# Performance work log

Hardware: AMD Instinct MI355X
Metric: run time of the kernel (lower is better)

Reference implementation:

```python
import jax, jax.numpy as jnp
import numpy as np

B, M, D, H = 8, 1024, 512, 8


def setup_inputs() -> dict:
    key = jax.random.key(0)
    ks = jax.random.split(key, 8)
    s = 0.02
    return {
        'x': jax.random.normal(ks[0], (B, M, D), jnp.float32),
        'scale': jnp.ones((M, D), jnp.float32),
        'Wq': jax.random.normal(ks[1], (H, D, D), jnp.float32) * s,
        'Wk': jax.random.normal(ks[2], (H, D, D), jnp.float32) * s,
        'Wv': jax.random.normal(ks[3], (H, D, D), jnp.float32) * s,
        'Wo': jax.random.normal(ks[4], (D, H * D), jnp.float32) * s,
        'bo': jnp.zeros((D,), jnp.float32),
        'Wff': jax.random.normal(ks[5], (D, D), jnp.float32) * s,
        'bff': jnp.zeros((D,), jnp.float32),
        'Wg': jax.random.normal(ks[6], (D, D), jnp.float32) * s,
        'bg': jnp.zeros((D,), jnp.float32),
        'Wl': jax.random.normal(ks[7], (D, D), jnp.float32) * s,
        'bl': jnp.zeros((D,), jnp.float32),
        'beta': jnp.ones((1,), jnp.float32),
    }


def _rope_cos_sin(m, d):
    # theta = 10000 ** (-2*(i-1)/d), faithful to the original (note the i-1 quirk)
    i = jnp.arange(d // 2, dtype=jnp.float32)
    theta = jnp.power(10000.0, -2.0 * (i - 1.0) / d)
    ang = jnp.arange(m, dtype=jnp.float32)[:, None] * theta[None, :]  # [m, d/2]
    return jnp.cos(ang), jnp.sin(ang)


def _apply_rope(t, cos, sin):
    # t: [..., m, d]; equivalent to bmm with the block-diagonal rotation matrix R[p]
    te, to = t[..., 0::2], t[..., 1::2]
    re = te * cos + to * sin
    ro = -te * sin + to * cos
    return jnp.stack([re, ro], axis=-1).reshape(t.shape)


def _rmsnorm(x, scale):
    b, m, d = x.shape
    ff_rms = jnp.sqrt(jnp.sum(x * x, axis=(1, 2))) * (m * d) ** (-0.5)  # [b]
    return scale[None, :m, :] * (x / ff_rms[:, None, None])


def reference(x, scale, Wq, Wk, Wv, Wo, bo, Wff, bff, Wg, bg, Wl, bl, beta):
    b, m, d = x.shape
    xn = _rmsnorm(x, scale)

    # per-head full-width projections (nn.Linear: y = x @ W.T)
    q = jnp.einsum('bmd,hod->hbmo', xn, Wq)  # [H,B,M,D]
    k = jnp.einsum('bmd,hod->hbmo', xn, Wk)
    v = jnp.einsum('bmd,hod->hbmo', xn, Wv)

    cos, sin = _rope_cos_sin(m, d)
    qr = _apply_rope(q, cos, sin)
    kr = _apply_rope(k, cos, sin)

    # SDPA with is_causal=False (no mask); dropout disabled (eval)
    scores = jnp.einsum('hbqd,hbkd->hbqk', qr, kr) / jnp.sqrt(jnp.float32(d))
    attn = jax.nn.softmax(scores, axis=-1)
    ctx = jnp.einsum('hbqk,hbkd->hbqd', attn, v)  # [H,B,M,D]

    cat = jnp.transpose(ctx, (1, 2, 0, 3)).reshape(b, m, -1)  # [B,M,H*D]
    attn_out = cat @ Wo.T + bo

    x2 = xn + attn_out
    x3 = _rmsnorm(x2, scale)

    h1 = x3 @ Wff.T + bff
    g = h1 @ Wg.T + bg
    sw = g * jax.nn.sigmoid(beta * g)
    ff = sw * (h1 @ Wl.T + bl)
    return x3 + ff
```

## Files before the change

kernel.cpp:

```cpp
#include <hip/hip_runtime.h>
#include <math.h>

typedef unsigned short u16;
typedef float f32x4 __attribute__((ext_vector_type(4)));
typedef __bf16 bf16x8 __attribute__((ext_vector_type(8)));
typedef unsigned short u16x8 __attribute__((ext_vector_type(8)));

__device__ __forceinline__ float bf2f(u16 u) {
    union { float f; unsigned int i; } v; v.i = ((unsigned int)u) << 16; return v.f;
}
__device__ __forceinline__ u16 f2bf(float f) {
    union { float f; unsigned int i; } v; v.f = f;
    unsigned int r = v.i + 0x7fffu + ((v.i >> 16) & 1u);
    return (u16)(r >> 16);
}
__device__ __forceinline__ float dpp_swap1(float v) {
    union { float f; int i; } a, b; a.f = v;
    b.i = __builtin_amdgcn_update_dpp(0, a.i, 0xB1, 0xF, 0xF, true);
    return b.f;
}

__device__ __forceinline__ void gll(const u16* g, u16* l) {
    __builtin_amdgcn_global_load_lds((const __attribute__((address_space(1))) void*)g,
                                     (__attribute__((address_space(3))) void*)l, 16, 0, 0);
}

struct EpiBF16 {
    u16* C; long zs; int ldc;
    __device__ void operator()(int z, int m, int n, float v) const {
        C[(long)z * zs + (long)m * ldc + n] = f2bf(v);
    }
};
struct EpiScale {
    u16* C; long zs; int ldc; float s;
    __device__ void operator()(int z, int m, int n, float v) const {
        C[(long)z * zs + (long)m * ldc + n] = f2bf(v * s);
    }
};
struct EpiAcc {
    float* x2;
    __device__ void operator()(int z, int m, int n, float v) const {
        x2[(long)m * 512 + n] += v;
    }
};
struct EpiBias16 {
    u16* C; const float* bias;
    __device__ void operator()(int z, int m, int n, float v) const {
        C[(long)m * 512 + n] = f2bf(v + bias[n]);
    }
};
struct EpiGL {
    u16* g; u16* l; const float* bg; const float* bl;
    __device__ void operator()(int z, int m, int n, float v) const {
        if (n < 512) g[(long)m * 512 + n] = f2bf(v + bg[n]);
        else         l[(long)m * 512 + n - 512] = f2bf(v + bl[n - 512]);
    }
};
struct EpiCtxMul {
    u16* C; const float* rs;
    __device__ void operator()(int z, int m, int n, float v) const {
        float r = __builtin_amdgcn_rcpf(rs[(long)z * 1024 + m]);
        C[(long)z * 524288 + (long)m * 512 + n] = f2bf(v * r);
    }
};

struct EpiScores {
    u16* C; float* rs; float sscale;
    __device__ float elem(int z, int m, int n, float v) const {
        float e = __expf(v * sscale);
        C[(long)z * 1048576 + (long)m * 1024 + n] = f2bf(e);
        return e;
    }
    __device__ void row(int z, int m, float p, int l15) const {
        p += __shfl_xor(p, 1, 64); p += __shfl_xor(p, 2, 64);
        p += __shfl_xor(p, 4, 64); p += __shfl_xor(p, 8, 64);
        if (l15 == 0) atomicAdd(rs + (long)z * 1024 + m, p);
    }
};
struct EpiAccA {
    float* x2;
    __device__ float elem(int z, int m, int n, float v) const {
        atomicAdd(x2 + (long)m * 512 + n, v);
        return 0.f;
    }
    __device__ void row(int, int, float, int) const {}
};

#define RDA(S, I) (*(const bf16x8*)(lds + (S) * 8192 + (I) * 512 + aro))
#define RDB(S, J) (*(const bf16x8*)(lds + (S) * 8192 + (J) * 512 + bro))
#define MFMA_PH(JP) do { \
    __builtin_amdgcn_s_barrier(); \
    asm volatile("s_waitcnt lgkmcnt(0)" ::: "memory"); \
    __builtin_amdgcn_sched_barrier(0); \
    __builtin_amdgcn_s_setprio(1); \
    _Pragma("unroll") \
    for (int i_ = 0; i_ < 8; i_++) { \
        acc[i_][2*(JP)]   = __builtin_amdgcn_mfma_f32_16x16x32_bf16(aF[i_], bF[0], acc[i_][2*(JP)], 0, 0, 0); \
        acc[i_][2*(JP)+1] = __builtin_amdgcn_mfma_f32_16x16x32_bf16(aF[i_], bF[1], acc[i_][2*(JP)+1], 0, 0, 0); \
    } \
    __builtin_amdgcn_s_setprio(0); \
} while (0)

__launch_bounds__(512, 2)
__global__ void gemm256_qkv(const u16* __restrict__ xnb, const u16* __restrict__ Wqkv,
                            u16* __restrict__ q, u16* __restrict__ k, u16* __restrict__ vT,
                            const float* __restrict__ csT) {
    __shared__ __align__(16) u16 lds[65536];
    const int t = threadIdx.x;
    const int lane = t & 63, wave = t >> 6;
    const int wr = wave >> 2, wc = wave & 3;
    const int l15 = lane & 15, quad = lane >> 4;
    const int sr = t >> 2;
    const int scw = ((t & 3) ^ ((t >> 3) & 3)) * 8;
    u16* lA0 = lds + wave * 512 + lane * 8;
    u16* lB0 = lds + 32768 + wave * 512 + lane * 8;
    const int ap = (quad ^ ((l15 >> 1) & 3)) * 8;
    const int aro = (wr * 128 + l15) * 32 + ap;
    const int bro = 32768 + (wc * 64 + l15) * 32 + ap;
    const int bid = blockIdx.x;

    const u16 *curA, *curB, *nxtA, *nxtB;
    int cm0, cn0, cz, cmode, nm0, nn0, nz, nmode;
    auto decode = [&](int tid, const u16*& A_, const u16*& B_,
                      int& m0_, int& n0_, int& z_, int& md_) {
        if (tid > 1535) tid = 1535;
        if (tid < 1024) {
            md_ = 0; z_ = tid & 15; int rem = tid >> 4;
            m0_ = (rem >> 1) << 8; n0_ = (rem & 1) << 8;
            A_ = xnb + (long)(m0_ + sr) * 512 + scw;
            B_ = Wqkv + z_ * 262144 + (long)(n0_ + sr) * 512 + scw;
        } else {
            int v = tid - 1024; md_ = 1; z_ = v & 7; int rem = v >> 3;
            m0_ = (rem & 1) << 8; n0_ = (rem >> 1) << 8;
            A_ = Wqkv + 4194304 + z_ * 262144 + (long)(m0_ + sr) * 512 + scw;
            B_ = xnb + (long)(n0_ + sr) * 512 + scw;
        }
    };
    decode(bid, curA, curB, cm0, cn0, cz, cmode);
    decode(bid + 256, nxtA, nxtB, nm0, nn0, nz, nmode);

    auto STGA = [&](int s) {
        const u16* base = (s < 16) ? curA : nxtA;
        int c = (s < 16) ? s : s - 16;
        u16* d = lA0 + (s & 3) * 8192;
        const u16* src = base + c * 32;
        gll(src, d); gll(src + 65536, d + 4096);
    };
    auto STGB = [&](int s) {
        const u16* base = (s < 16) ? curB : nxtB;
        int c = (s < 16) ? s : s - 16;
        u16* d = lB0 + (s & 3) * 8192;
        const u16* src = base + c * 32;
        gll(src, d); gll(src + 65536, d + 4096);
    };

    STGA(0); STGB(0); STGA(1); STGB(1); STGA(2); STGB(2);
    asm volatile("s_waitcnt vmcnt(4)" ::: "memory");
    __builtin_amdgcn_s_barrier();

    for (int j = 0; j < 6; ++j) {
        f32x4 acc[8][4] = {};
        #pragma unroll
        for (int it = 0; it < 4; ++it) {
            const int sh = 3 + it * 4;
            bf16x8 aF[8], bF[2];
            #pragma unroll
            for (int i = 0; i < 8; i++) aF[i] = RDA(0, i);
            bF[0] = RDB(0, 0); bF[1] = RDB(0, 1);
            STGA(sh);
            MFMA_PH(0);
            __builtin_amdgcn_s_barrier();
            bF[0] = RDB(0, 2); bF[1] = RDB(0, 3);
            STGB(sh);
            MFMA_PH(1);
            __builtin_amdgcn_s_barrier();
            #pragma unroll
            for (int i = 0; i < 8; i++) aF[i] = RDA(1, i);
            bF[0] = RDB(1, 0); bF[1] = RDB(1, 1);
            STGA(sh + 1);
            MFMA_PH(0);
            __builtin_amdgcn_s_barrier();
            bF[0] = RDB(1, 2); bF[1] = RDB(1, 3);
            STGB(sh + 1);
            MFMA_PH(1);
            asm volatile("s_waitcnt vmcnt(4)" ::: "memory");
            __builtin_amdgcn_s_barrier();
            #pragma unroll
            for (int i = 0; i < 8; i++) aF[i] = RDA(2, i);
            bF[0] = RDB(2, 0); bF[1] = RDB(2, 1);
            STGA(sh + 2);
            MFMA_PH(0);
            __builtin_amdgcn_s_barrier();
            bF[0] = RDB(2, 2); bF[1] = RDB(2, 3);
            STGB(sh + 2);
            MFMA_PH(1);
            __builtin_amdgcn_s_barrier();
            #pragma unroll
            for (int i = 0; i < 8; i++) aF[i] = RDA(3, i);
            bF[0] = RDB(3, 0); bF[1] = RDB(3, 1);
            STGA(sh + 3);
            MFMA_PH(0);
            __builtin_amdgcn_s_barrier();
            bF[0] = RDB(3, 2); bF[1] = RDB(3, 3);
            STGB(sh + 3);
            MFMA_PH(1);
            asm volatile("s_waitcnt vmcnt(4)" ::: "memory");
            __builtin_amdgcn_s_barrier();
        }
        if (cmode == 0) {
            u16* dst = ((cz >= 8) ? k : q) + ((long)(cz & 7) << 22);
            const int odd = l15 & 1;
            #pragma unroll
            for (int i = 0; i < 8; i++)
                #pragma unroll
                for (int r = 0; r < 4; r++) {
                    int m = cm0 + wr * 128 + i * 16 + quad * 4 + r;
                    const float* cs = csT + (long)(m & 1023) * 512;
                    #pragma unroll
                    for (int jj = 0; jj < 4; jj++) {
                        int n = cn0 + wc * 64 + jj * 16 + l15;
                        float val = acc[i][jj][r];
                        float pv = dpp_swap1(val);
                        float c = cs[(n >> 1) * 2], s = cs[(n >> 1) * 2 + 1];
                        float o = odd ? (val * c - pv * s) : (val * c + pv * s);
                        dst[(long)m * 512 + n] = f2bf(o);
                    }
                }
        } else {
            #pragma unroll
            for (int i = 0; i < 8; i++)
                #pragma unroll
                for (int r = 0; r < 4; r++) {
                    int m = cm0 + wr * 128 + i * 16 + quad * 4 + r;
                    #pragma unroll
                    for (int jj = 0; jj < 4; jj++) {
                        int n = cn0 + wc * 64 + jj * 16 + l15;
                        vT[((long)cz << 22) + ((long)(n >> 10) << 19) + ((long)m << 10) + (n & 1023)]
                            = f2bf(acc[i][jj][r]);
                    }
                }
        }
        curA = nxtA; curB = nxtB; cm0 = nm0; cn0 = nn0; cz = nz; cmode = nmode;
        decode(bid + (j + 2) * 256, nxtA, nxtB, nm0, nn0, nz, nmode);
    }
    asm volatile("s_waitcnt vmcnt(0)" ::: "memory");
}

template <class Epi>
__launch_bounds__(512, 2)
__global__ void gemm256(const u16* __restrict__ A, const u16* __restrict__ B,
                        int nkh, int kssh, int lda, int ldb,
                        long aBatch, long bBatch, long aSeg, long bSeg, Epi epi) {
    __shared__ __align__(16) u16 lds[65536];
    const int t = threadIdx.x;
    const int lane = t & 63, wave = t >> 6;
    const int wr = wave >> 2, wc = wave & 3;
    const int l15 = lane & 15, quad = lane >> 4;
    const int m0 = blockIdx.x * 256, n0 = blockIdx.y * 256;
    const int z = blockIdx.z;
    const int sr = t >> 2;
    const int scw = ((t & 3) ^ ((t >> 3) & 3)) * 8;
    const u16* gA = A + (long)z * aBatch + (long)(m0 + sr) * lda + scw;
    const u16* gB = B + (long)z * bBatch + (long)(n0 + sr) * ldb + scw;
    const long a128 = 128L * lda, b128 = 128L * ldb;
    u16* lA0 = lds + wave * 512 + lane * 8;
    u16* lB0 = lds + 32768 + wave * 512 + lane * 8;
    const int kmask = (1 << kssh) - 1;

    auto STA = [&](int shp) {
        int c = shp < nkh ? shp : nkh - 1;
        const u16* s = gA + (long)(c >> kssh) * aSeg + (c & kmask) * 32;
        u16* d = lA0 + (shp & 3) * 8192;
        gll(s, d); gll(s + a128, d + 4096);
    };
    auto STB = [&](int shp) {
        int c = shp < nkh ? shp : nkh - 1;
        const u16* s = gB + (long)(c >> kssh) * bSeg + (c & kmask) * 32;
        u16* d = lB0 + (shp & 3) * 8192;
        gll(s, d); gll(s + b128, d + 4096);
    };

    const int ap = (quad ^ ((l15 >> 1) & 3)) * 8;
    const int aro = (wr * 128 + l15) * 32 + ap;
    const int bro = 32768 + (wc * 64 + l15) * 32 + ap;
    f32x4 acc[8][4] = {};

    STA(0); STB(0); STA(1); STB(1); STA(2); STB(2);
    asm volatile("s_waitcnt vmcnt(4)" ::: "memory");
    __builtin_amdgcn_s_barrier();

    const int niter = nkh >> 2;
    int sh = 3;
    for (int it = 0; it < niter; it++) {
        bf16x8 aF[8], bF[2];
        #pragma unroll
        for (int i = 0; i < 8; i++) aF[i] = RDA(0, i);
        bF[0] = RDB(0, 0); bF[1] = RDB(0, 1);
        STA(sh);
        MFMA_PH(0);
        __builtin_amdgcn_s_barrier();
        bF[0] = RDB(0, 2); bF[1] = RDB(0, 3);
        STB(sh);
        MFMA_PH(1);
        __builtin_amdgcn_s_barrier();
        #pragma unroll
        for (int i = 0; i < 8; i++) aF[i] = RDA(1, i);
        bF[0] = RDB(1, 0); bF[1] = RDB(1, 1);
        STA(sh + 1);
        MFMA_PH(0);
        __builtin_amdgcn_s_barrier();
        bF[0] = RDB(1, 2); bF[1] = RDB(1, 3);
        STB(sh + 1);
        MFMA_PH(1);
        asm volatile("s_waitcnt vmcnt(4)" ::: "memory");
        __builtin_amdgcn_s_barrier();
        #pragma unroll
        for (int i = 0; i < 8; i++) aF[i] = RDA(2, i);
        bF[0] = RDB(2, 0); bF[1] = RDB(2, 1);
        STA(sh + 2);
        MFMA_PH(0);
        __builtin_amdgcn_s_barrier();
        bF[0] = RDB(2, 2); bF[1] = RDB(2, 3);
        STB(sh + 2);
        MFMA_PH(1);
        __builtin_amdgcn_s_barrier();
        #pragma unroll
        for (int i = 0; i < 8; i++) aF[i] = RDA(3, i);
        bF[0] = RDB(3, 0); bF[1] = RDB(3, 1);
        STA(sh + 3);
        MFMA_PH(0);
        __builtin_amdgcn_s_barrier();
        bF[0] = RDB(3, 2); bF[1] = RDB(3, 3);
        STB(sh + 3);
        MFMA_PH(1);
        asm volatile("s_waitcnt vmcnt(4)" ::: "memory");
        __builtin_amdgcn_s_barrier();
        sh += 4;
    }
    asm volatile("s_waitcnt vmcnt(0)" ::: "memory");

    #pragma unroll
    for (int i = 0; i < 8; i++)
        #pragma unroll
        for (int r = 0; r < 4; r++) {
            int m = m0 + wr * 128 + i * 16 + quad * 4 + r;
            float p = 0.f;
            #pragma unroll
            for (int j = 0; j < 4; j++)
                p += epi.elem(z, m, n0 + wc * 64 + j * 16 + l15, acc[i][j][r]);
            epi.row(z, m, p, l15);
        }
}
#undef RDA
#undef RDB
#undef MFMA_PH

template <class Epi>
__launch_bounds__(256, 4)
__global__ void gemm128(const u16* __restrict__ A, const u16* __restrict__ B,
                        int Kseg, int nSeg, int lda, int ldb,
                        long aBatch, long bBatch, long aSeg, Epi epi) {
    __shared__ __align__(16) u16 sA[8192];
    __shared__ __align__(16) u16 sB[8192];
    const int t = threadIdx.x;
    const int lane = t & 63, wave = t >> 6;
    const int wr = wave >> 1, wc = wave & 1;
    const int l15 = lane & 15, quad = lane >> 4;
    const int m0 = blockIdx.x * 128, n0 = blockIdx.y * 128;
    const int sr = t >> 2;
    const int scw = ((t & 3) ^ ((t >> 3) & 3)) * 8;
    const u16* gA = A + (long)blockIdx.z * aBatch + (long)(m0 + sr) * lda + scw;
    const u16* gB = B + (long)blockIdx.z * bBatch + (long)(n0 + sr) * ldb + scw;
    const long a2 = 64L * lda, b2 = 64L * ldb;
    u16* lA = sA + wave * 512 + lane * 8;
    u16* lB = sB + wave * 512 + lane * 8;
    const int ap = (quad ^ ((l15 >> 1) & 3)) * 8;
    const int ab = (wr * 64 + l15) * 32 + ap;
    const int bb = (wc * 64 + l15) * 32 + ap;
    f32x4 acc[4][4] = {};
    for (int s = 0; s < nSeg; s++) {
        const u16* gAs = gA + (long)s * aSeg;
        const u16* gBs = gB + s * Kseg;
        for (int k0 = 0; k0 < Kseg; k0 += 64) {
            gll(gAs + k0, lA);             gll(gAs + k0 + a2, lA + 2048);
            gll(gBs + k0, lB);             gll(gBs + k0 + b2, lB + 2048);
            gll(gAs + k0 + 32, lA + 4096); gll(gAs + k0 + 32 + a2, lA + 6144);
            gll(gBs + k0 + 32, lB + 4096); gll(gBs + k0 + 32 + b2, lB + 6144);
            __syncthreads();
            #pragma unroll
            for (int half = 0; half < 2; half++) {
                bf16x8 aF[4], bF[4];
                #pragma unroll
                for (int i = 0; i < 4; i++) aF[i] = *(const bf16x8*)(sA + half * 4096 + ab + i * 512);
                #pragma unroll
                for (int j = 0; j < 4; j++) bF[j] = *(const bf16x8*)(sB + half * 4096 + bb + j * 512);
                #pragma unroll
                for (int i = 0; i < 4; i++)
                    #pragma unroll
                    for (int j = 0; j < 4; j++)
                        acc[i][j] = __builtin_amdgcn_mfma_f32_16x16x32_bf16(aF[i], bF[j], acc[i][j], 0, 0, 0);
            }
            __syncthreads();
        }
    }
    #pragma unroll
    for (int i = 0; i < 4; i++)
        #pragma unroll
        for (int j = 0; j < 4; j++)
            #pragma unroll
            for (int r = 0; r < 4; r++)
                epi(blockIdx.z, m0 + wr * 64 + i * 16 + quad * 4 + r,
                    n0 + wc * 64 + j * 16 + l15, acc[i][j][r]);
}

__device__ __forceinline__ float waveSum(float v) {
    #pragma unroll
    for (int o = 32; o > 0; o >>= 1) v += __shfl_down(v, o, 64);
    return v;
}
__device__ __forceinline__ float invFromPart(const float* part, int b) {
    float s = part[b * 64 + (threadIdx.x & 63)];
    s = waveSum(s);
    s = __shfl(s, 0, 64);
    return sqrtf(524288.0f / s);
}

__global__ void sumsq_f32(const float* __restrict__ x, float* __restrict__ part) {
    __shared__ float tmp[4];
    long base = (long)blockIdx.x * 524288 + (long)blockIdx.y * 8192;
    float s = 0.f;
    for (int i = threadIdx.x; i < 8192; i += 256) { float v = x[base + i]; s += v * v; }
    s = waveSum(s);
    if ((threadIdx.x & 63) == 0) tmp[threadIdx.x >> 6] = s;
    __syncthreads();
    if (threadIdx.x == 0) part[blockIdx.x * 64 + blockIdx.y] = tmp[0] + tmp[1] + tmp[2] + tmp[3];
}
__global__ void finalize_inv(const float* __restrict__ part, float* __restrict__ inv) {
    float s = part[blockIdx.x * 64 + threadIdx.x];
    s = waveSum(s);
    if (threadIdx.x == 0) inv[blockIdx.x] = sqrtf(524288.0f / s);
}
__global__ void rmsnorm1f_a(const float* __restrict__ x, const float* __restrict__ scale,
                            const float* __restrict__ part, const float* __restrict__ bo,
                            u16* __restrict__ xnb, float* __restrict__ x2) {
    long i = (long)blockIdx.x * 256 + threadIdx.x;
    int b = (int)(i >> 19), md = (int)(i & 524287);
    float inv = invFromPart(part, b);
    float v = x[i] * inv * scale[md];
    xnb[i] = f2bf(v);
    x2[i] = v + bo[i & 511];
}
__global__ void rmsnorm2_a(const float* __restrict__ x2, const float* __restrict__ scale,
                           const float* __restrict__ part, u16* __restrict__ x3b) {
    long i = (long)blockIdx.x * 256 + threadIdx.x;
    int b = (int)(i >> 19), md = (int)(i & 524287);
    float inv = invFromPart(part, b);
    x3b[i] = f2bf(x2[i] * inv * scale[md]);
}
__global__ void final_out_a(const float* __restrict__ x2, const float* __restrict__ scale,
                            const float* __restrict__ part, const u16* __restrict__ g,
                            const u16* __restrict__ l, const float* __restrict__ beta,
                            float* __restrict__ out) {
    long i = (long)blockIdx.x * 256 + threadIdx.x;
    int b = (int)(i >> 19), md = (int)(i & 524287);
    float inv2 = invFromPart(part, b);
    float x3 = x2[i] * inv2 * scale[md];
    float gv = bf2f(g[i]), lv = bf2f(l[i]);
    float bta = beta[0];
    float sw = gv / (1.0f + expf(-bta * gv));
    out[i] = x3 + sw * lv;
}
__global__ void rmsnorm1f(const float* __restrict__ x, const float* __restrict__ scale,
                          const float* __restrict__ inv, const float* __restrict__ bo,
                          u16* __restrict__ xnb, float* __restrict__ x2) {
    long i = (long)blockIdx.x * 256 + threadIdx.x;
    int b = (int)(i >> 19), md = (int)(i & 524287);
    float v = x[i] * inv[b] * scale[md];
    xnb[i] = f2bf(v);
    x2[i] = v + bo[i & 511];
}
__global__ void rmsnorm2(const float* __restrict__ x2, const float* __restrict__ scale,
                         const float* __restrict__ inv, u16* __restrict__ x3b) {
    long i = (long)blockIdx.x * 256 + threadIdx.x;
    int b = (int)(i >> 19), md = (int)(i & 524287);
    x3b[i] = f2bf(x2[i] * inv[b] * scale[md]);
}
__global__ void final_out(const float* __restrict__ x2, const float* __restrict__ scale,
                          const float* __restrict__ inv2, const u16* __restrict__ g,
                          const u16* __restrict__ l, const float* __restrict__ beta,
                          float* __restrict__ out) {
    long i = (long)blockIdx.x * 256 + threadIdx.x;
    int b = (int)(i >> 19), md = (int)(i & 524287);
    float x3 = x2[i] * inv2[b] * scale[md];
    float gv = bf2f(g[i]), lv = bf2f(l[i]);
    float bta = beta[0];
    float sw = gv / (1.0f + expf(-bta * gv));
    out[i] = x3 + sw * lv;
}
__global__ void rope_tables_a(float* __restrict__ csT, float* __restrict__ rowsum) {
    int i = blockIdx.x * 256 + threadIdx.x;
    int m = i >> 8, j = i & 255;
    float theta = powf(10000.0f, -2.0f * ((float)j - 1.0f) / 512.0f);
    float ang = (float)m * theta;
    csT[2 * i] = cosf(ang); csT[2 * i + 1] = sinf(ang);
    if (i < 65536) rowsum[i] = 0.f;
}
__global__ void rope_tables(float* __restrict__ cosT, float* __restrict__ sinT) {
    int i = blockIdx.x * 256 + threadIdx.x;
    int m = i >> 8, j = i & 255;
    float theta = powf(10000.0f, -2.0f * ((float)j - 1.0f) / 512.0f);
    float ang = (float)m * theta;
    cosT[i] = cosf(ang); sinT[i] = sinf(ang);
}
__global__ void rope_apply(u16* __restrict__ tq, const float* __restrict__ cosT,
                           const float* __restrict__ sinT) {
    long i = (long)blockIdx.x * 256 + threadIdx.x;
    int j = (int)(i & 255), m = (int)((i >> 8) & 1023);
    float c = cosT[m * 256 + j], s = sinT[m * 256 + j];
    long base = i * 2;
    float te = bf2f(tq[base]), to = bf2f(tq[base + 1]);
    tq[base]     = f2bf(te * c + to * s);
    tq[base + 1] = f2bf(-te * s + to * c);
}
__global__ void transpose_v(const u16* __restrict__ v, u16* __restrict__ vT) {
    __shared__ u16 tile[32][33];
    long zb = (long)blockIdx.z * 524288;
    int mo = blockIdx.x * 32, oo = blockIdx.y * 32;
    int tx = threadIdx.x & 31, ty = threadIdx.x >> 5;
    for (int r = ty; r < 32; r += 8) tile[r][tx] = v[zb + (long)(mo + r) * 512 + oo + tx];
    __syncthreads();
    for (int r = ty; r < 32; r += 8) vT[zb + (long)(oo + r) * 1024 + mo + tx] = tile[tx][r];
}
__launch_bounds__(256)
__global__ void softmax_rows4(u16* __restrict__ sc) {
    int row = blockIdx.x * 4 + (threadIdx.x >> 6);
    int lane = threadIdx.x & 63;
    u16* p = sc + (long)row * 1024 + lane * 16;
    float v[16]; float mx = -1e30f;
    #pragma unroll
    for (int i = 0; i < 16; i++) { v[i] = bf2f(p[i]); mx = fmaxf(mx, v[i]); }
    #pragma unroll
    for (int o = 32; o > 0; o >>= 1) mx = fmaxf(mx, __shfl_xor(mx, o, 64));
    float s = 0.f;
    #pragma unroll
    for (int i = 0; i < 16; i++) { v[i] = expf(v[i] - mx); s += v[i]; }
    #pragma unroll
    for (int o = 32; o > 0; o >>= 1) s += __shfl_xor(s, o, 64);
    float r = 1.0f / s;
    #pragma unroll
    for (int i = 0; i < 16; i++) p[i] = f2bf(v[i] * r);
}
__device__ __forceinline__ void cvt8(const float* __restrict__ s, u16* __restrict__ d) {
    f32x4 a = *(const f32x4*)s, b = *(const f32x4*)(s + 4);
    u16x8 o;
    o[0] = f2bf(a[0]); o[1] = f2bf(a[1]); o[2] = f2bf(a[2]); o[3] = f2bf(a[3]);
    o[4] = f2bf(b[0]); o[5] = f2bf(b[1]); o[6] = f2bf(b[2]); o[7] = f2bf(b[3]);
    *(u16x8*)d = o;
}
__global__ void prep_w(const float* __restrict__ Wq, const float* __restrict__ Wk,
                       const float* __restrict__ Wv, const float* __restrict__ Wo,
                       const float* __restrict__ Wff, const float* __restrict__ Wg,
                       const float* __restrict__ Wl,
                       u16* __restrict__ Wqkvb, u16* __restrict__ Wob,
                       u16* __restrict__ Wffb, u16* __restrict__ Wglb) {
    long i = ((long)blockIdx.x * 256 + threadIdx.x) * 8;
    if (i < 2097152)      cvt8(Wq + i, Wqkvb + i);
    else if (i < 4194304) cvt8(Wk + (i - 2097152), Wqkvb + i);
    else if (i < 6291456) cvt8(Wv + (i - 4194304), Wqkvb + i);
    else if (i < 8388608) cvt8(Wo + (i - 6291456), Wob + (i - 6291456));
    else if (i < 8650752) cvt8(Wff + (i - 8388608), Wffb + (i - 8388608));
    else if (i < 8912896) cvt8(Wg + (i - 8650752), Wglb + (i - 8650752));
    else                  cvt8(Wl + (i - 8912896), Wglb + 262144 + (i - 8912896));
}
__global__ void convert_f2b(const float* __restrict__ s, u16* __restrict__ d, int n) {
    int i = blockIdx.x * 256 + threadIdx.x;
    if (i < n) d[i] = f2bf(s[i]);
}
__global__ void convert3(const float* __restrict__ a, const float* __restrict__ b,
                         const float* __restrict__ c, u16* __restrict__ d) {
    int i = blockIdx.x * 256 + threadIdx.x;
    const float* s = (i < 262144) ? a : (i < 524288) ? b : c;
    d[i] = f2bf(s[i & 262143]);
}

#define MB 1048576L
extern "C" void kernel_launch(void* const* d_in, const int* in_sizes, int n_in,
                              void* d_out, int out_size, void* d_ws, size_t ws_size,
                              hipStream_t stream) {
    (void)in_sizes; (void)n_in; (void)out_size;
    const float* x    = (const float*)d_in[0];
    const float* scale= (const float*)d_in[1];
    const float* Wq   = (const float*)d_in[2];
    const float* Wk   = (const float*)d_in[3];
    const float* Wv   = (const float*)d_in[4];
    const float* Wo   = (const float*)d_in[5];
    const float* bo   = (const float*)d_in[6];
    const float* Wff  = (const float*)d_in[7];
    const float* bff  = (const float*)d_in[8];
    const float* Wg   = (const float*)d_in[9];
    const float* bg   = (const float*)d_in[10];
    const float* Wl   = (const float*)d_in[11];
    const float* bl   = (const float*)d_in[12];
    const float* beta = (const float*)d_in[13];
    float* out = (float*)d_out;
    char* ws = (char*)d_ws;
    const float sscale = 0.044194173824159216f;

    if (ws_size >= 260000000UL) {
        u16*   xnb   = (u16*)  (ws);
        u16*   q_all = (u16*)  (ws + 8*MB);
        u16*   k_all = (u16*)  (ws + 72*MB);
        u16*   vT_all= (u16*)  (ws + 136*MB);
        u16*   sc    = (u16*)  (ws + 200*MB);
        u16*   Wqkvb = (u16*)  (ws + 200*MB);
        u16*   Wob   = (u16*)  (ws + 232*MB);
        u16*   Wffb  = (u16*)  (ws + 236*MB);
        u16*   Wglb  = (u16*)  (ws + 236*MB + 524288L);
        float* csT   = (float*)(ws + 237*MB + 1572864L);
        float* rowsum= (float*)(ws + 239*MB + 1572864L);
        float* part  = (float*)(ws + 239*MB + 1835008L);
        float* x2    = out;
        u16* x3b = k_all; u16* h1 = k_all + 4194304; u16* g = k_all + 8388608; u16* l = k_all + 12582912;

        sumsq_f32<<<dim3(8, 64), 256, 0, stream>>>(x, part);
        rmsnorm1f_a<<<16384, 256, 0, stream>>>(x, scale, part, bo, xnb, x2);
        rope_tables_a<<<1024, 256, 0, stream>>>(csT, rowsum);
        prep_w<<<4480, 256, 0, stream>>>(Wq, Wk, Wv, Wo, Wff, Wg, Wl,
                                         Wqkvb, Wob, Wffb, Wglb);

        gemm256_qkv<<<256, 512, 0, stream>>>(xnb, Wqkvb, q_all, k_all, vT_all, csT);

        for (int h0 = 0; h0 < 8; h0 += 2) {
            const long off = (long)h0 * 4194304;
            float* rsc = rowsum + (long)h0 * 8192;
            gemm256<<<dim3(4, 4, 16), 512, 0, stream>>>(q_all + off, k_all + off, 16, 4, 512, 512,
                524288L, 524288L, 512L, 512L, EpiScores{sc, rsc, sscale});
            gemm128<<<dim3(8, 4, 16), 256, 0, stream>>>(sc, vT_all + off, 1024, 1, 1024, 1024,
                1048576L, 524288L, 0L, EpiCtxMul{q_all + off, rsc});
        }
        gemm256<<<dim3(32, 2, 4), 512, 0, stream>>>(q_all, Wob, 32, 4, 512, 4096,
            8388608L, 1024L, 4194304L, 512L, EpiAccA{x2});

        sumsq_f32<<<dim3(8, 64), 256, 0, stream>>>(x2, part);
        rmsnorm2_a<<<16384, 256, 0, stream>>>(x2, scale, part, x3b);

        gemm128<<<dim3(64, 4, 1), 256, 0, stream>>>(x3b, Wffb, 512, 1, 512, 512,
            0L, 0L, 0L, EpiBias16{h1, bff});
        gemm128<<<dim3(64, 8, 1), 256, 0, stream>>>(h1, Wglb, 512, 1, 512, 512,
            0L, 0L, 0L, EpiGL{g, l, bg, bl});
        final_out_a<<<16384, 256, 0, stream>>>(x2, scale, part, g, l, beta, out);
        return;
    }

    u16*   xnb  = (u16*)  (ws);
    float* x2   = (float*)(ws + 8388608L);
    u16*   qh   = (u16*)  (ws + 25165824L);
    u16*   kh   = (u16*)  (ws + 33554432L);
    u16*   vhc  = (u16*)  (ws + 41943040L);
    u16*   vT   = (u16*)  (ws + 50331648L);
    u16*   Whb  = (u16*)  (ws + 58720256L);
    u16*   Wob  = (u16*)  (ws + 60293120L);
    u16*   Wfb  = (u16*)  (ws + 64487424L);
    u16*   Wgb  = (u16*)  (ws + 65011712L);
    u16*   Wlb  = (u16*)  (ws + 65536000L);
    float* cosT = (float*)(ws + 66060288L);
    float* sinT = (float*)(ws + 67108864L);
    float* part = (float*)(ws + 68157440L);
    float* inv1 = (float*)(ws + 68159488L);
    float* inv2 = (float*)(ws + 68159552L);
    u16*   sc   = (u16*)  (ws + 68159616L);
    u16*   x3b = qh;  u16* h1 = kh;  u16* g = vhc;  u16* l = vT;
    const bool big = ws_size >= 85002240UL;

    sumsq_f32<<<dim3(8, 64), 256, 0, stream>>>(x, part);
    finalize_inv<<<8, 64, 0, stream>>>(part, inv1);
    rmsnorm1f<<<16384, 256, 0, stream>>>(x, scale, inv1, bo, xnb, x2);
    rope_tables<<<1024, 256, 0, stream>>>(cosT, sinT);
    convert_f2b<<<8192, 256, 0, stream>>>(Wo, Wob, 2097152);
    convert_f2b<<<1024, 256, 0, stream>>>(Wff, Wfb, 262144);
    convert_f2b<<<1024, 256, 0, stream>>>(Wg, Wgb, 262144);
    convert_f2b<<<1024, 256, 0, stream>>>(Wl, Wlb, 262144);

    for (int h = 0; h < 8; h++) {
        convert3<<<3072, 256, 0, stream>>>(Wq + (long)h * 262144, Wk + (long)h * 262144,
                                           Wv + (long)h * 262144, Whb);
        gemm128<<<dim3(64, 4, 3), 256, 0, stream>>>(xnb, Whb, 512, 1, 512, 512, 0L, 262144L, 0L,
                                                    EpiBF16{qh, 4194304L, 512});
        rope_apply<<<16384, 256, 0, stream>>>(qh, cosT, sinT);
        transpose_v<<<dim3(32, 16, 8), 256, 0, stream>>>(vhc, vT);
        if (big) {
            gemm128<<<dim3(8, 8, 8), 256, 0, stream>>>(qh, kh, 512, 1, 512, 512, 524288L, 524288L,
                                                       0L, EpiScale{sc, 1048576L, 1024, sscale});
            softmax_rows4<<<2048, 256, 0, stream>>>(sc);
            gemm128<<<dim3(8, 4, 8), 256, 0, stream>>>(sc, vT, 1024, 1, 1024, 1024, 1048576L,
                                                       524288L, 0L, EpiBF16{vhc, 524288L, 512});
        } else {
            for (int b = 0; b < 8; b++) {
                gemm128<<<dim3(8, 8, 1), 256, 0, stream>>>(qh + (long)b * 524288, kh + (long)b * 524288,
                                                           512, 1, 512, 512, 0L, 0L, 0L,
                                                           EpiScale{sc, 0L, 1024, sscale});
                softmax_rows4<<<256, 256, 0, stream>>>(sc);
                gemm128<<<dim3(8, 4, 1), 256, 0, stream>>>(sc, vT + (long)b * 524288, 1024, 1, 1024,
                                                           1024, 0L, 0L, 0L,
                                                           EpiBF16{vhc + (long)b * 524288, 0L, 512});
            }
        }
        gemm128<<<dim3(64, 4, 1), 256, 0, stream>>>(vhc, Wob + (long)h * 512, 512, 1, 512, 4096,
                                                    0L, 0L, 0L, EpiAcc{x2});
    }

    sumsq_f32<<<dim3(8, 64), 256, 0, stream>>>(x2, part);
    finalize_inv<<<8, 64, 0, stream>>>(part, inv2);
    rmsnorm2<<<16384, 256, 0, stream>>>(x2, scale, inv2, x3b);
    gemm128<<<dim3(64, 4, 1), 256, 0, stream>>>(x3b, Wfb, 512, 1, 512, 512, 0L, 0L, 0L,
                                                EpiBias16{h1, bff});
    gemm128<<<dim3(64, 4, 1), 256, 0, stream>>>(h1, Wgb, 512, 1, 512, 512, 0L, 0L, 0L,
                                                EpiBias16{g, bg});
    gemm128<<<dim3(64, 4, 1), 256, 0, stream>>>(h1, Wlb, 512, 1, 512, 512, 0L, 0L, 0L,
                                                EpiBias16{l, bl});
    final_out<<<16384, 256, 0, stream>>>(x2, scale, inv2, g, l, beta, out);
}
```

Measured before the change: 643.1 us.

## Pack GEMM epilogue stores, replace atomic split-K with partials, vectorize elementwise kernels

GEMM epilogues now pair adjacent columns with a DPP swap, so even lanes write two bf16 values (or two floats) as one 32/64-bit store instead of two scalar stores. The Wo split-K GEMM writes per-split partial buffers instead of doing float atomicAdds into x2. A new combine kernel sums those partials into x2 and computes the sum of squares in the same pass, which removes the separate sumsq launch. The rmsnorm and final elementwise kernels process four elements per thread with vector loads and a fast exp. The cost is an extra 64MB partial buffer written and read back, and a reused k_all region.

```diff
diff --git a/kernel.cpp b/kernel.cpp
--- a/kernel.cpp
+++ b/kernel.cpp
@@ -2,8 +2,10 @@
 #include <math.h>
 
 typedef unsigned short u16;
+typedef float f32x2 __attribute__((ext_vector_type(2)));
 typedef float f32x4 __attribute__((ext_vector_type(4)));
 typedef __bf16 bf16x8 __attribute__((ext_vector_type(8)));
+typedef unsigned short u16x4 __attribute__((ext_vector_type(4)));
 typedef unsigned short u16x8 __attribute__((ext_vector_type(8)));
 
 __device__ __forceinline__ float bf2f(u16 u) {
@@ -18,6 +20,9 @@
     union { float f; int i; } a, b; a.f = v;
     b.i = __builtin_amdgcn_update_dpp(0, a.i, 0xB1, 0xF, 0xF, true);
     return b.f;
+}
+__device__ __forceinline__ unsigned int pack2(float lo, float hi) {
+    return (unsigned int)f2bf(lo) | ((unsigned int)f2bf(hi) << 16);
 }
 
 __device__ __forceinline__ void gll(const u16* g, u16* l) {
@@ -60,7 +65,10 @@
     u16* C; const float* rs;
     __device__ void operator()(int z, int m, int n, float v) const {
         float r = __builtin_amdgcn_rcpf(rs[(long)z * 1024 + m]);
-        C[(long)z * 524288 + (long)m * 512 + n] = f2bf(v * r);
+        float o = v * r;
+        float po = dpp_swap1(o);
+        if (!(n & 1))
+            *(unsigned int*)(C + (long)z * 524288 + (long)m * 512 + n) = pack2(o, po);
     }
 };
 
@@ -68,7 +76,9 @@
     u16* C; float* rs; float sscale;
     __device__ float elem(int z, int m, int n, float v) const {
         float e = __expf(v * sscale);
-        C[(long)z * 1048576 + (long)m * 1024 + n] = f2bf(e);
+        float pe = dpp_swap1(e);
+        if (!(n & 1))
+            *(unsigned int*)(C + (long)z * 1048576 + (long)m * 1024 + n) = pack2(e, pe);
         return e;
     }
     __device__ void row(int z, int m, float p, int l15) const {
@@ -77,10 +87,14 @@
         if (l15 == 0) atomicAdd(rs + (long)z * 1024 + m, p);
     }
 };
-struct EpiAccA {
-    float* x2;
+struct EpiPart {
+    float* p;
     __device__ float elem(int z, int m, int n, float v) const {
-        atomicAdd(x2 + (long)m * 512 + n, v);
+        float pv = dpp_swap1(v);
+        if (!(n & 1)) {
+            f32x2 o; o[0] = v; o[1] = pv;
+            *(f32x2*)(p + (long)z * 4194304 + (long)m * 512 + n) = o;
+        }
         return 0.f;
     }
     __device__ void row(int, int, float, int) const {}
@@ -118,6 +132,7 @@
     const int aro = (wr * 128 + l15) * 32 + ap;
     const int bro = 32768 + (wc * 64 + l15) * 32 + ap;
     const int bid = blockIdx.x;
+    const bool evn = !(l15 & 1);
 
     const u16 *curA, *curB, *nxtA, *nxtB;
     int cm0, cn0, cz, cmode, nm0, nn0, nz, nmode;
@@ -209,7 +224,6 @@
         }
         if (cmode == 0) {
             u16* dst = ((cz >= 8) ? k : q) + ((long)(cz & 7) << 22);
-            const int odd = l15 & 1;
             #pragma unroll
             for (int i = 0; i < 8; i++)
                 #pragma unroll
@@ -221,9 +235,12 @@
                         int n = cn0 + wc * 64 + jj * 16 + l15;
                         float val = acc[i][jj][r];
                         float pv = dpp_swap1(val);
-                        float c = cs[(n >> 1) * 2], s = cs[(n >> 1) * 2 + 1];
-                        float o = odd ? (val * c - pv * s) : (val * c + pv * s);
-                        dst[(long)m * 512 + n] = f2bf(o);
+                        if (evn) {
+                            f32x2 c2 = *(const f32x2*)(cs + n);
+                            float oe = val * c2[0] + pv * c2[1];
+                            float oo = pv * c2[0] - val * c2[1];
+                            *(unsigned int*)(dst + (long)m * 512 + n) = pack2(oe, oo);
+                        }
                     }
                 }
         } else {
@@ -235,8 +252,11 @@
                     #pragma unroll
                     for (int jj = 0; jj < 4; jj++) {
                         int n = cn0 + wc * 64 + jj * 16 + l15;
-                        vT[((long)cz << 22) + ((long)(n >> 10) << 19) + ((long)m << 10) + (n & 1023)]
-                            = f2bf(acc[i][jj][r]);
+                        float val = acc[i][jj][r];
+                        float pv = dpp_swap1(val);
+                        if (evn)
+                            *(unsigned int*)(vT + ((long)cz << 22) + ((long)(n >> 10) << 19)
+                                             + ((long)m << 10) + (n & 1023)) = pack2(val, pv);
                     }
                 }
         }
@@ -429,12 +449,34 @@
     __shared__ float tmp[4];
     long base = (long)blockIdx.x * 524288 + (long)blockIdx.y * 8192;
     float s = 0.f;
-    for (int i = threadIdx.x; i < 8192; i += 256) { float v = x[base + i]; s += v * v; }
+    for (int i = threadIdx.x * 4; i < 8192; i += 1024) {
+        f32x4 v = *(const f32x4*)(x + base + i);
+        s += v[0] * v[0] + v[1] * v[1] + v[2] * v[2] + v[3] * v[3];
+    }
     s = waveSum(s);
     if ((threadIdx.x & 63) == 0) tmp[threadIdx.x >> 6] = s;
     __syncthreads();
     if (threadIdx.x == 0) part[blockIdx.x * 64 + blockIdx.y] = tmp[0] + tmp[1] + tmp[2] + tmp[3];
 }
+__global__ void combine_x2(float* __restrict__ x2, const float* __restrict__ p,
+                           float* __restrict__ part) {
+    __shared__ float tmp[4];
+    long base = (long)blockIdx.x * 524288 + (long)blockIdx.y * 8192;
+    float s = 0.f;
+    for (int i = threadIdx.x * 4; i < 8192; i += 1024) {
+        f32x4 v = *(const f32x4*)(x2 + base + i);
+        v = v + *(const f32x4*)(p + base + i);
+        v = v + *(const f32x4*)(p + 4194304 + base + i);
+        v = v + *(const f32x4*)(p + 8388608 + base + i);
+        v = v + *(const f32x4*)(p + 12582912 + base + i);
+        *(f32x4*)(x2 + base + i) = v;
+        s += v[0] * v[0] + v[1] * v[1] + v[2] * v[2] + v[3] * v[3];
+    }
+    s = waveSum(s);
+    if ((threadIdx.x & 63) == 0) tmp[threadIdx.x >> 6] = s;
+    __syncthreads();
+    if (threadIdx.x == 0) part[blockIdx.x * 64 + blockIdx.y] = tmp[0] + tmp[1] + tmp[2] + tmp[3];
+}
 __global__ void finalize_inv(const float* __restrict__ part, float* __restrict__ inv) {
     float s = part[blockIdx.x * 64 + threadIdx.x];
     s = waveSum(s);
@@ -443,32 +485,51 @@
 __global__ void rmsnorm1f_a(const float* __restrict__ x, const float* __restrict__ scale,
                             const float* __restrict__ part, const float* __restrict__ bo,
                             u16* __restrict__ xnb, float* __restrict__ x2) {
-    long i = (long)blockIdx.x * 256 + threadIdx.x;
-    int b = (int)(i >> 19), md = (int)(i & 524287);
+    long i = ((long)blockIdx.x * 256 + threadIdx.x) * 4;
+    int b = (int)(i >> 19);
     float inv = invFromPart(part, b);
-    float v = x[i] * inv * scale[md];
-    xnb[i] = f2bf(v);
-    x2[i] = v + bo[i & 511];
+    f32x4 xv = *(const f32x4*)(x + i);
+    f32x4 sv = *(const f32x4*)(scale + (int)(i & 524287));
+    f32x4 bv = *(const f32x4*)(bo + (int)(i & 511));
+    f32x4 v; u16x4 o;
+    #pragma unroll
+    for (int j = 0; j < 4; j++) { v[j] = xv[j] * inv * sv[j]; o[j] = f2bf(v[j]); }
+    *(u16x4*)(xnb + i) = o;
+    *(f32x4*)(x2 + i) = v + bv;
 }
 __global__ void rmsnorm2_a(const float* __restrict__ x2, const float* __restrict__ scale,
                            const float* __restrict__ part, u16* __restrict__ x3b) {
-    long i = (long)blockIdx.x * 256 + threadIdx.x;
-    int b = (int)(i >> 19), md = (int)(i & 524287);
+    long i = ((long)blockIdx.x * 256 + threadIdx.x) * 4;
+    int b = (int)(i >> 19);
     float inv = invFromPart(part, b);
-    x3b[i] = f2bf(x2[i] * inv * scale[md]);
+    f32x4 xv = *(const f32x4*)(x2 + i);
+    f32x4 sv = *(const f32x4*)(scale + (int)(i & 524287));
+    u16x4 o;
+    #pragma unroll
+    for (int j = 0; j < 4; j++) o[j] = f2bf(xv[j] * inv * sv[j]);
+    *(u16x4*)(x3b + i) = o;
 }
 __global__ void final_out_a(const float* __restrict__ x2, const float* __restrict__ scale,
                             const float* __restrict__ part, const u16* __restrict__ g,
                             const u16* __restrict__ l, const float* __restrict__ beta,
                             float* __restrict__ out) {
-    long i = (long)blockIdx.x * 256 + threadIdx.x;
-    int b = (int)(i >> 19), md = (int)(i & 524287);
+    long i = ((long)blockIdx.x * 256 + threadIdx.x) * 4;
+    int b = (int)(i >> 19);
     float inv2 = invFromPart(part, b);
-    float x3 = x2[i] * inv2 * scale[md];
-    float gv = bf2f(g[i]), lv = bf2f(l[i]);
     float bta = beta[0];
-    float sw = gv / (1.0f + expf(-bta * gv));
-    out[i] = x3 + sw * lv;
+    f32x4 xv = *(const f32x4*)(x2 + i);
+    f32x4 sv = *(const f32x4*)(scale + (int)(i & 524287));
+    u16x4 gv4 = *(const u16x4*)(g + i);
+    u16x4 lv4 = *(const u16x4*)(l + i);
+    f32x4 o;
+    #pragma unroll
+    for (int j = 0; j < 4; j++) {
+        float x3 = xv[j] * inv2 * sv[j];
+        float gv = bf2f(gv4[j]), lv = bf2f(lv4[j]);
+        float sw = gv / (1.0f + __expf(-bta * gv));
+        o[j] = x3 + sw * lv;
+    }
+    *(f32x4*)(out + i) = o;
 }
 __global__ void rmsnorm1f(const float* __restrict__ x, const float* __restrict__ scale,
                           const float* __restrict__ inv, const float* __restrict__ bo,
@@ -620,10 +681,11 @@
         float* rowsum= (float*)(ws + 239*MB + 1572864L);
         float* part  = (float*)(ws + 239*MB + 1835008L);
         float* x2    = out;
+        float* wop   = (float*)k_all;
         u16* x3b = k_all; u16* h1 = k_all + 4194304; u16* g = k_all + 8388608; u16* l = k_all + 12582912;
 
         sumsq_f32<<<dim3(8, 64), 256, 0, stream>>>(x, part);
-        rmsnorm1f_a<<<16384, 256, 0, stream>>>(x, scale, part, bo, xnb, x2);
+        rmsnorm1f_a<<<4096, 256, 0, stream>>>(x, scale, part, bo, xnb, x2);
         rope_tables_a<<<1024, 256, 0, stream>>>(csT, rowsum);
         prep_w<<<4480, 256, 0, stream>>>(Wq, Wk, Wv, Wo, Wff, Wg, Wl,
                                          Wqkvb, Wob, Wffb, Wglb);
@@ -639,16 +701,15 @@
                 1048576L, 524288L, 0L, EpiCtxMul{q_all + off, rsc});
         }
         gemm256<<<dim3(32, 2, 4), 512, 0, stream>>>(q_all, Wob, 32, 4, 512, 4096,
-            8388608L, 1024L, 4194304L, 512L, EpiAccA{x2});
-
-        sumsq_f32<<<dim3(8, 64), 256, 0, stream>>>(x2, part);
-        rmsnorm2_a<<<16384, 256, 0, stream>>>(x2, scale, part, x3b);
+            8388608L, 1024L, 4194304L, 512L, EpiPart{wop});
+        combine_x2<<<dim3(8, 64), 256, 0, stream>>>(x2, wop, part);
+        rmsnorm2_a<<<4096, 256, 0, stream>>>(x2, scale, part, x3b);
 
         gemm128<<<dim3(64, 4, 1), 256, 0, stream>>>(x3b, Wffb, 512, 1, 512, 512,
             0L, 0L, 0L, EpiBias16{h1, bff});
         gemm128<<<dim3(64, 8, 1), 256, 0, stream>>>(h1, Wglb, 512, 1, 512, 512,
             0L, 0L, 0L, EpiGL{g, l, bg, bl});
-        final_out_a<<<16384, 256, 0, stream>>>(x2, scale, part, g, l, beta, out);
+        final_out_a<<<4096, 256, 0, stream>>>(x2, scale, part, g, l, beta, out);
         return;
     }
 
```

New measurement: 733.1 us. 1.14x slower.
